# Optimization experiments

Measured on AMD Instinct MI355X. Metric: run time of the kernel, lower is better.

## Reference

```python
import jax, jax.numpy as jnp
import numpy as np
from jax import lax

ORDER = 6
WN = 0.5 / 50.0          # highpass_cutoff / (orig_fs/2)
UP, DOWN = 16, 25        # 64/100 reduced by gcd 4 (scipy resample_poly)
HALF_LEN = 10 * DOWN     # scipy kaiser half length = 10*max_rate
NTAPS = 2 * HALF_LEN + 1
PADLEN = 21              # sosfiltfilt default: 3*(2*n_sections+1), 3 biquads
CHANNELS = np.array([126, 125, 48, 112, 67, 93, 10, 61, 39, 108])
D_MODEL = 16
LN_EPS = 1e-5


def _butter_hp_sos(order, wn):
    # scipy.signal.butter(order, wn, btype='high', output='sos') in pure numpy
    fs = 2.0
    warped = 2.0 * fs * np.tan(np.pi * wn / fs)
    m = np.arange(-order + 1, order, 2)
    p = -np.exp(1j * np.pi * m / (2 * order))     # analog LP prototype poles
    k = np.real(1.0 / np.prod(-p))                # lp2hp gain (no zeros)
    p = warped / p                                # lp2hp poles; zeros at s=0
    z = np.zeros(order)
    fs2 = 2.0 * fs                                # bilinear, fs=2
    k = k * np.real(np.prod(fs2 - z) / np.prod(fs2 - p))
    z = (fs2 + z) / (fs2 - z)                     # digital zeros, all +1
    p = (fs2 + p) / (fs2 - p)
    pp = p[np.imag(p) > 0]
    pp = pp[np.argsort(-np.abs(np.abs(pp) - 1.0))]  # closest to unit circle last
    sos = []
    for i, pi in enumerate(pp):
        b = np.array([1.0, -2.0, 1.0]) * (k if i == 0 else 1.0)
        a = np.array([1.0, -2.0 * pi.real, np.abs(pi) ** 2])
        sos.append(np.concatenate([b, a]))
    return np.array(sos)


def _sosfilt_zi(sos):
    # scipy.signal.sosfilt_zi: steady-state of step response per section
    n = sos.shape[0]
    zi = np.zeros((n, 2))
    scale = 1.0
    for s in range(n):
        b0, b1, b2, _, a1, a2 = sos[s]
        A = np.array([[1.0 + a1, -1.0], [a2, 1.0]])
        B = np.array([b1 - a1 * b0, b2 - a2 * b0])
        zi[s] = scale * np.linalg.solve(A, B)
        scale *= (b0 + b1 + b2) / (1.0 + a1 + a2)
    return zi


SOS = _butter_hp_sos(ORDER, WN)
ZI = _sosfilt_zi(SOS)


def _resample_fir():
    # scipy firwin(2*half_len+1, 1/max_rate, window=('kaiser',5.0)) * up
    fc = 1.0 / DOWN
    m = np.arange(NTAPS) - (NTAPS - 1) / 2.0
    h = fc * np.sinc(fc * m) * np.kaiser(NTAPS, 5.0)
    h /= h.sum()
    return h * UP


H_BASE = _resample_fir()


def _pos_encoding(max_len, d):
    pos = np.arange(max_len)[:, None].astype(np.float64)
    div = np.exp(np.arange(0, d, 2) * (-np.log(10000.0) / d))
    pe = np.zeros((max_len, d))
    pe[:, 0::2] = np.sin(pos * div)
    pe[:, 1::2] = np.cos(pos * div)
    return pe.astype(np.float32)


PE = _pos_encoding(3840, D_MODEL)


def _sosfilt(x, zi):
    # x: (N,T), zi: (N,3,2). Cascade of biquads, transposed direct form II.
    sos = jnp.asarray(SOS, x.dtype)
    nsec = SOS.shape[0]

    def step(z, xt):
        v = xt
        zs = []
        for s in range(nsec):  # fixed tiny cascade, unrolled inside scan
            b0, b1, b2, a1, a2 = sos[s, 0], sos[s, 1], sos[s, 2], sos[s, 4], sos[s, 5]
            y = b0 * v + z[s][0]
            zs.append((b1 * v - a1 * y + z[s][1], b2 * v - a2 * y))
            v = y
        return tuple(zs), v

    z0 = tuple((zi[:, s, 0], zi[:, s, 1]) for s in range(nsec))
    _, y = lax.scan(step, z0, x.T)
    return y.T


def _sosfiltfilt(x):
    # scipy.signal.sosfiltfilt with default odd padding, padlen=21
    zi = jnp.asarray(ZI, x.dtype)
    front = 2.0 * x[:, :1] - x[:, PADLEN:0:-1]
    back = 2.0 * x[:, -1:] - x[:, -2:-PADLEN - 2:-1]
    ext = jnp.concatenate([front, x, back], axis=1)
    y = _sosfilt(ext, zi[None] * ext[:, 0, None, None])
    y = y[:, ::-1]
    y = _sosfilt(y, zi[None] * y[:, 0, None, None])
    return y[:, ::-1][:, PADLEN:-PADLEN]


def _resample_poly(x):
    # scipy.signal.resample_poly(x, 64, 100): upfirdn via dilated conv
    T = x.shape[-1]
    n_out = (T * UP) // DOWN + int((T * UP) % DOWN != 0)
    n_pre_pad = DOWN - HALF_LEN % DOWN
    n_pre_remove = (HALF_LEN + n_pre_pad) // DOWN

    def outlen(lh):
        return (((T - 1) * UP + lh) - 1) // DOWN + 1

    n_post = 0
    while outlen(NTAPS + n_pre_pad + n_post) < n_out + n_pre_remove:
        n_post += 1
    h = np.concatenate([np.zeros(n_pre_pad), H_BASE, np.zeros(n_post)])
    L = h.size
    rhs = jnp.asarray(h[::-1].copy(), x.dtype).reshape(1, 1, L)
    y = lax.conv_general_dilated(x[:, None, :], rhs, window_strides=(DOWN,),
                                 padding=[(L - 1, L - 1)], lhs_dilation=(UP,),
                                 dimension_numbers=('NCH', 'OIH', 'NCH'))
    return y[:, 0, n_pre_remove:n_pre_remove + n_out]


def _ln(x, g, b):
    mu = x.mean(-1, keepdims=True)
    var = ((x - mu) ** 2).mean(-1, keepdims=True)
    return (x - mu) * lax.rsqrt(var + LN_EPS) * g + b


def setup_inputs() -> dict:
    key = jax.random.key(0)
    ks = jax.random.split(key, 20)
    f32 = jnp.float32
    d = {
        'x': jax.random.normal(ks[0], (64, 128, 2000), f32),
        'conv_w': jax.random.normal(ks[1], (16, 10, 3), f32) * 0.15,
        'conv_b': jnp.zeros((16,), f32),
        'ln0_g': jnp.ones((16,), f32), 'ln0_b': jnp.zeros((16,), f32),
        'wqkv': jax.random.normal(ks[2], (48, 16), f32) * 0.125,
        'bqkv': jnp.zeros((48,), f32),
        'wo': jax.random.normal(ks[3], (16, 16), f32) * 0.25,
        'bo': jnp.zeros((16,), f32),
        'w1': jax.random.normal(ks[4], (32, 16), f32) * 0.2,
        'b1': jnp.zeros((32,), f32),
        'w2': jax.random.normal(ks[5], (16, 32), f32) * 0.2,
        'b2': jnp.zeros((16,), f32),
        'ln1_g': jnp.ones((16,), f32), 'ln1_b': jnp.zeros((16,), f32),
        'ln2_g': jnp.ones((16,), f32), 'ln2_b': jnp.zeros((16,), f32),
        'wfc': jax.random.normal(ks[6], (1, 16), f32) * 0.3,
        'bfc': jnp.zeros((1,), f32),
    }
    return d


def reference(x, conv_w, conv_b, ln0_g, ln0_b, wqkv, bqkv, wo, bo,
              w1, b1, w2, b2, ln1_g, ln1_b, ln2_g, ln2_b, wfc, bfc):
    B = x.shape[0]
    # remove Cz (last channel) then gather interesting channels
    x = x[:, :-1, :][:, jnp.asarray(CHANNELS), :]        # (B,10,T)
    x = x - x.mean(axis=1, keepdims=True)                # CAR
    C, T = x.shape[1], x.shape[2]
    xf = _sosfiltfilt(x.reshape(B * C, T))               # zero-phase highpass
    xr = _resample_poly(xf)                              # 100 Hz -> 64 Hz
    x = xr.reshape(B, C, -1)
    x = jnp.tanh(x)                                      # artifact_scale = 1.0
    mean = x.mean(axis=2, keepdims=True)                 # zscore, unbiased std
    var = ((x - mean) ** 2).sum(axis=2, keepdims=True) / (x.shape[2] - 1)
    std = jnp.maximum(jnp.sqrt(var), 1e-6)
    x = (x - mean) / std
    # conv1d k=3 pad=1 (10 -> 16) + relu
    x = lax.conv_general_dilated(x, conv_w, (1,), [(1, 1)],
                                 dimension_numbers=('NCH', 'OIH', 'NCH'))
    x = jax.nn.relu(x + conv_b[None, :, None])
    x = x.transpose(0, 2, 1)                             # (B,S,16)
    x = _ln(x, ln0_g, ln0_b)
    x = x + jnp.asarray(PE[:x.shape[1]], x.dtype)[None]
    # TransformerEncoderLayer, post-norm, nhead=1, relu FFN (eval: no dropout)
    qkv = x @ wqkv.T + bqkv
    q, k, v = jnp.split(qkv, 3, axis=-1)
    att = jax.nn.softmax(jnp.einsum('bqd,bkd->bqk', q, k) * 0.25, axis=-1)
    a = jnp.einsum('bqk,bkd->bqd', att, v) @ wo.T + bo
    x = _ln(x + a, ln1_g, ln1_b)
    f = jax.nn.relu(x @ w1.T + b1) @ w2.T + b2
    x = _ln(x + f, ln2_g, ln2_b)
    pooled = x.mean(axis=1)                              # adaptive avg pool -> 1
    return pooled @ wfc.T + bfc                          # (B,1)
```

## Files before the change

kernel.cpp:

```cpp
#include <hip/hip_runtime.h>
#include <cmath>
#include <complex>
#include <algorithm>

#ifndef M_PI
#define M_PI 3.14159265358979323846
#endif

typedef _Float16 f16x8 __attribute__((ext_vector_type(8)));
typedef _Float16 f16x4 __attribute__((ext_vector_type(4)));
typedef float f32x4 __attribute__((ext_vector_type(4)));

struct FiltArg {
  double b0[3], b1[3], b2[3], a1[3], a2[3];
  double zi0[3], zi1[3];
};
struct CorArg { double CA[16 * 6]; };
struct EigArg {
  double Pm[36], Pinv[36];
  double czi[6];
  double lam_re[3], lam_im[3];
  double lami_re[3], lami_im[3];
};
struct FirArg { float h[526]; };

static void design_sos(FiltArg& sa) {
  const int order = 6;
  const double wn = 0.5 / 50.0;
  const double fs = 2.0;
  double warped = 2.0 * fs * std::tan(M_PI * wn / fs);
  std::complex<double> p[6];
  for (int i = 0; i < order; i++) {
    int m = -order + 1 + 2 * i;
    p[i] = -std::exp(std::complex<double>(0.0, M_PI * m / (2.0 * order)));
  }
  std::complex<double> prod1(1, 0);
  for (int i = 0; i < 6; i++) prod1 *= -p[i];
  double k = (1.0 / prod1).real();
  for (int i = 0; i < 6; i++) p[i] = warped / p[i];
  const double fs2 = 2.0 * fs;
  std::complex<double> num(1, 0), den(1, 0);
  for (int i = 0; i < 6; i++) { num *= fs2; den *= (fs2 - p[i]); }
  k *= (num / den).real();
  for (int i = 0; i < 6; i++) p[i] = (fs2 + p[i]) / (fs2 - p[i]);
  std::complex<double> pp[3]; int n = 0;
  for (int i = 0; i < 6; i++) if (p[i].imag() > 0) pp[n++] = p[i];
  std::stable_sort(pp, pp + 3,
    [](const std::complex<double>& A, const std::complex<double>& B) {
      return std::fabs(std::abs(A) - 1.0) > std::fabs(std::abs(B) - 1.0);
    });
  double sos[3][6];
  for (int s = 0; s < 3; s++) {
    double g = (s == 0) ? k : 1.0;
    sos[s][0] = g; sos[s][1] = -2.0 * g; sos[s][2] = g;
    sos[s][3] = 1.0; sos[s][4] = -2.0 * pp[s].real(); sos[s][5] = std::norm(pp[s]);
  }
  double scale = 1.0;
  for (int s = 0; s < 3; s++) {
    double b0 = sos[s][0], b1 = sos[s][1], b2 = sos[s][2];
    double a1 = sos[s][4], a2 = sos[s][5];
    double det = 1.0 + a1 + a2;
    double r0 = b1 - a1 * b0, r1 = b2 - a2 * b0;
    double z0 = (r0 + r1) / det;
    double z1 = ((1.0 + a1) * r1 - a2 * r0) / det;
    sa.b0[s] = b0; sa.b1[s] = b1; sa.b2[s] = b2; sa.a1[s] = a1; sa.a2[s] = a2;
    sa.zi0[s] = scale * z0; sa.zi1[s] = scale * z1;
    scale *= (b0 + b1 + b2) / (1.0 + a1 + a2);
  }
}

static double host_step(const FiltArg& c, double z[6], double v) {
  for (int s = 0; s < 3; s++) {
    double y = c.b0[s] * v + z[2 * s];
    z[2 * s]     = c.b1[s] * v - c.a1[s] * y + z[2 * s + 1];
    z[2 * s + 1] = c.b2[s] * v - c.a2[s] * y;
    v = y;
  }
  return v;
}

static void build_filt(FiltArg& c, CorArg& co) {
  design_sos(c);
  for (int j = 0; j < 6; j++) {
    double z[6] = {0, 0, 0, 0, 0, 0};
    z[j] = 1.0;
    for (int i = 0; i < 16; i++) co.CA[i * 6 + j] = host_step(c, z, 0.0);
  }
}

static void build_eig(const FiltArg& c, EigArg& e) {
  double Pr[36];
  for (int s = 0; s < 3; s++) {
    double a1 = c.a1[s], a2 = c.a2[s];
    std::complex<double> disc = std::sqrt(std::complex<double>(a1 * a1 - 4.0 * a2, 0.0));
    std::complex<double> p = (-a1 + disc) / 2.0;
    if (p.imag() < 0) p = std::conj(p);
    std::complex<double> v[6] = {0, 0, 0, 0, 0, 0};
    v[2 * s] = 1.0;
    v[2 * s + 1] = a1 + p;
    std::complex<double> y = 1.0;
    for (int j = s + 1; j < 3; j++) {
      double b0j = c.b0[j], b1j = c.b1[j], b2j = c.b2[j];
      double a1j = c.a1[j], a2j = c.a2[j];
      std::complex<double> det = p * p + a1j * p + a2j;
      std::complex<double> r0 = (b1j - a1j * b0j) * y;
      std::complex<double> r1 = (b2j - a2j * b0j) * y;
      std::complex<double> z0 = (p * r0 + r1) / det;
      std::complex<double> z1 = ((p + a1j) * r1 - a2j * r0) / det;
      v[2 * j] = z0; v[2 * j + 1] = z1;
      y = b0j * y + z0;
    }
    for (int i = 0; i < 6; i++) {
      Pr[i * 6 + 2 * s]     = v[i].real();
      Pr[i * 6 + 2 * s + 1] = v[i].imag();
    }
    std::complex<double> lam = std::pow(p, 16);
    e.lam_re[s] = lam.real(); e.lam_im[s] = lam.imag();
    std::complex<double> li = 1.0 / lam;
    e.lami_re[s] = li.real(); e.lami_im[s] = li.imag();
  }
  for (int i = 0; i < 36; i++) e.Pm[i] = Pr[i];
  double M[6][12];
  for (int i = 0; i < 6; i++)
    for (int j = 0; j < 6; j++) { M[i][j] = Pr[i * 6 + j]; M[i][6 + j] = (i == j) ? 1.0 : 0.0; }
  for (int col = 0; col < 6; col++) {
    int piv = col;
    for (int i = col + 1; i < 6; i++)
      if (std::fabs(M[i][col]) > std::fabs(M[piv][col])) piv = i;
    if (piv != col) for (int j = 0; j < 12; j++) std::swap(M[col][j], M[piv][j]);
    double d = M[col][col];
    for (int j = 0; j < 12; j++) M[col][j] /= d;
    for (int i = 0; i < 6; i++) if (i != col) {
      double f = M[i][col];
      for (int j = 0; j < 12; j++) M[i][j] -= f * M[col][j];
    }
  }
  for (int i = 0; i < 6; i++)
    for (int j = 0; j < 6; j++) e.Pinv[i * 6 + j] = M[i][6 + j];
  double zv[6];
  for (int s = 0; s < 3; s++) { zv[2 * s] = c.zi0[s]; zv[2 * s + 1] = c.zi1[s]; }
  for (int i = 0; i < 6; i++) {
    double sum = 0.0;
    for (int j = 0; j < 6; j++) sum += e.Pinv[i * 6 + j] * zv[j];
    e.czi[i] = sum;
  }
}

static double bessel_i0(double x) {
  double s = 1.0, t = 1.0;
  for (int k = 1; k < 64; k++) {
    double u = x / (2.0 * k);
    t *= u * u; s += t;
    if (t < 1e-18 * s) break;
  }
  return s;
}

static void design_fir(FirArg& fa) {
  double h[501];
  const double fc = 1.0 / 25.0;
  double denom = bessel_i0(5.0);
  double sum = 0.0;
  for (int nn = 0; nn < 501; nn++) {
    double m = nn - 250.0;
    double xx = fc * m;
    double snc = (nn == 250) ? 1.0 : std::sin(M_PI * xx) / (M_PI * xx);
    double r = (2.0 * nn) / 500.0 - 1.0;
    double w = bessel_i0(5.0 * std::sqrt(std::max(0.0, 1.0 - r * r))) / denom;
    h[nn] = fc * snc * w; sum += h[nn];
  }
  for (int nn = 0; nn < 25; nn++) fa.h[nn] = 0.0f;
  for (int nn = 0; nn < 501; nn++) fa.h[25 + nn] = (float)(h[nn] / sum * 16.0);
}

__device__ inline double waveReduceSum(double v) {
  #pragma unroll
  for (int off = 32; off > 0; off >>= 1) v += __shfl_down(v, off, 64);
  return v;
}

__device__ inline void cpow_int(double br, double bi, int n, double& rr_, double& ri_) {
  double rr = 1.0, ri = 0.0;
  while (n) {
    if (n & 1) { double t = rr * br - ri * bi; ri = rr * bi + ri * br; rr = t; }
    double t2 = br * br - bi * bi; bi = 2.0 * br * bi; br = t2;
    n >>= 1;
  }
  rr_ = rr; ri_ = ri;
}

__global__ __launch_bounds__(256) void k_chansel_pe(const float* __restrict__ x,
                                                    float* __restrict__ xs,
                                                    float* __restrict__ pe,
                                                    float* __restrict__ out) {
  int gid = blockIdx.x;
  if (gid < 500) {
    int idx = gid * 256 + threadIdx.x;
    int b = idx / 2000, t = idx % 2000;
    const int ch[10] = {126, 125, 48, 112, 67, 93, 10, 61, 39, 108};
    const float* xb = x + (size_t)b * 128 * 2000;
    float v[10]; float s = 0.f;
    #pragma unroll
    for (int c = 0; c < 10; c++) { v[c] = xb[ch[c] * 2000 + t]; s += v[c]; }
    s *= 0.1f;
    #pragma unroll
    for (int c = 0; c < 10; c++) xs[((size_t)b * 10 + c) * 2000 + t] = v[c] - s;
  } else {
    int i = (gid - 500) * 256 + threadIdx.x;
    int t = i >> 4, d = i & 15, j = d >> 1;
    double div = exp(-((double)(2 * j)) * 0.5756462732485114);
    double a = (double)t * div;
    pe[i] = (float)((d & 1) ? cos(a) : sin(a));
    if (gid == 579 && threadIdx.x < 64) out[threadIdx.x] = 0.f;
  }
}

#define XR(t) xr[(t) + ((t) >> 5)]
#define YF(t) yf[(t) + ((t) >> 5)]
__global__ __launch_bounds__(128) void k_filtfilt(float* __restrict__ xs,
                                                  FiltArg c, CorArg co, EigArg eg) {
  __shared__ float xr[2112];
  __shared__ double yf[2112];
  __shared__ double wsum[3][2];
  int r = blockIdx.x;
  int gk = threadIdx.x;
  int lane = gk & 63;
  int wv = gk >> 6;
  float* x = xs + (size_t)r * 2000;

  float x0f = x[0], xlf = x[1999];
  for (int t = gk; t < 2048; t += 128) {
    float v;
    if (t < 21)        v = 2.f * x0f - x[21 - t];
    else if (t < 2021) v = x[t - 21];
    else if (t < 2042) v = 2.f * xlf - x[4019 - t];
    else               v = 0.f;
    XR(t) = v;
  }
  __syncthreads();

  double b0[3], b1[3], b2[3], a1[3], a2[3];
  #pragma unroll
  for (int s = 0; s < 3; s++) {
    b0[s] = c.b0[s]; b1[s] = c.b1[s]; b2[s] = c.b2[s];
    a1[s] = c.a1[s]; a2[s] = c.a2[s];
  }
  auto step = [&](double* z, double v) -> double {
    #pragma unroll
    for (int s = 0; s < 3; s++) {
      double y = b0[s] * v + z[2 * s];
      z[2 * s]     = b1[s] * v - a1[s] * y + z[2 * s + 1];
      z[2 * s + 1] = b2[s] * v - a2[s] * y;
      v = y;
    }
    return v;
  };

  auto eigscan = [&](double seed, const double* F, double* zst) {
    double G[6];
    #pragma unroll
    for (int i = 0; i < 6; i++) {
      double s = 0.0;
      #pragma unroll
      for (int j = 0; j < 6; j++) s += eg.Pinv[i * 6 + j] * F[j];
      G[i] = s;
    }
    double tre[3], tim[3], sre[3], sim[3];
    #pragma unroll
    for (int s3 = 0; s3 < 3; s3++) {
      double gre = G[2 * s3], gim = -G[2 * s3 + 1];
      double mre, mim;
      cpow_int(eg.lami_re[s3], eg.lami_im[s3], gk, mre, mim);
      tre[s3] = mre * gre - mim * gim;
      tim[s3] = mre * gim + mim * gre;
      double pr = tre[s3], pi = tim[s3];
      #pragma unroll
      for (int off = 1; off < 64; off <<= 1) {
        double ore = __shfl_up(pr, off, 64);
        double oim = __shfl_up(pi, off, 64);
        pr += (lane >= off) ? ore : 0.0;
        pi += (lane >= off) ? oim : 0.0;
      }
      sre[s3] = pr; sim[s3] = pi;
      if (wv == 0 && lane == 63) { wsum[s3][0] = pr; wsum[s3][1] = pi; }
    }
    __syncthreads();
    double coord[6];
    #pragma unroll
    for (int s3 = 0; s3 < 3; s3++) {
      double inc_re = sre[s3] + (wv ? wsum[s3][0] : 0.0);
      double inc_im = sim[s3] + (wv ? wsum[s3][1] : 0.0);
      double Sre = inc_re - tre[s3], Sim = inc_im - tim[s3];
      double c0re = seed * eg.czi[2 * s3];
      double c0im = -seed * eg.czi[2 * s3 + 1];
      double lkre, lkim;
      cpow_int(eg.lam_re[s3], eg.lam_im[s3], gk, lkre, lkim);
      double lm1re = lkre * eg.lami_re[s3] - lkim * eg.lami_im[s3];
      double lm1im = lkre * eg.lami_im[s3] + lkim * eg.lami_re[s3];
      if (gk == 0) { lm1re = 0.0; lm1im = 0.0; }
      double cre = lkre * c0re - lkim * c0im + lm1re * Sre - lm1im * Sim;
      double cim = lkre * c0im + lkim * c0re + lm1re * Sim + lm1im * Sre;
      coord[2 * s3] = cre;
      coord[2 * s3 + 1] = -cim;
    }
    #pragma unroll
    for (int i = 0; i < 6; i++) {
      double s = 0.0;
      #pragma unroll
      for (int j = 0; j < 6; j++) s += eg.Pm[i * 6 + j] * coord[j];
      zst[i] = s;
    }
  };

  int t0 = gk * 16;
  double z[6], yreg[16], zst[6];

  #pragma unroll
  for (int i = 0; i < 6; i++) z[i] = 0.0;
  for (int i = 0; i < 16; i++) yreg[i] = step(z, (double)XR(t0 + i));
  eigscan((double)XR(0), z, zst);
  for (int i = 0; i < 16; i++) {
    double corr = 0.0;
    #pragma unroll
    for (int j = 0; j < 6; j++) corr += co.CA[i * 6 + j] * zst[j];
    YF(t0 + i) = yreg[i] + corr;
  }
  __syncthreads();

  auto rin = [&](int j) -> double { return (j <= 2041) ? YF(2041 - j) : 0.0; };
  double seedB = YF(2041);
  #pragma unroll
  for (int i = 0; i < 6; i++) z[i] = 0.0;
  for (int i = 0; i < 16; i++) yreg[i] = step(z, rin(t0 + i));
  eigscan(seedB, z, zst);
  for (int i = 0; i < 16; i++) {
    int j = t0 + i;
    if (j >= 21 && j <= 2020) {
      double corr = 0.0;
      #pragma unroll
      for (int jj = 0; jj < 6; jj++) corr += co.CA[i * 6 + jj] * zst[jj];
      x[2020 - j] = (float)(yreg[i] + corr);
    }
  }
}

__global__ __launch_bounds__(256) void k_resample_norm(const float* __restrict__ xf,
                                                       float* __restrict__ xn,
                                                       FirArg fa) {
  __shared__ float xl[2000];
  __shared__ float hl[526];
  int r = blockIdx.x;
  const float* x = xf + (size_t)r * 2000;
  for (int i = threadIdx.x; i < 2000; i += 256) xl[i] = x[i];
  for (int i = threadIdx.x; i < 526; i += 256) hl[i] = fa.h[i];
  __syncthreads();
  float vals[5];
  #pragma unroll
  for (int kk = 0; kk < 5; kk++) {
    int o = threadIdx.x + kk * 256;
    int P = 25 * (o + 11);
    int phase = P & 15;
    float acc = 0.f;
    for (int m = phase; m <= 525; m += 16) {
      int idx = (P - m) >> 4;
      if (idx >= 0 && idx < 2000) acc += hl[m] * xl[idx];
    }
    vals[kk] = tanhf(acc);
  }
  double s = 0.0, ss = 0.0;
  #pragma unroll
  for (int kk = 0; kk < 5; kk++) {
    s += (double)vals[kk]; ss += (double)vals[kk] * (double)vals[kk];
  }
  s = waveReduceSum(s); ss = waveReduceSum(ss);
  __shared__ double red[8];
  int wid = threadIdx.x >> 6, lane = threadIdx.x & 63;
  if (lane == 0) { red[wid] = s; red[4 + wid] = ss; }
  __syncthreads();
  double S = red[0] + red[1] + red[2] + red[3];
  double SS = red[4] + red[5] + red[6] + red[7];
  double mean = S / 1280.0;
  double var = (SS - 1280.0 * mean * mean) / 1279.0;
  double sd = fmax(sqrt(fmax(var, 0.0)), 1e-6);
  float fmean = (float)mean, finv = (float)(1.0 / sd);
  #pragma unroll
  for (int kk = 0; kk < 5; kk++)
    xn[(size_t)r * 1280 + threadIdx.x + kk * 256] = (vals[kk] - fmean) * finv;
}

__global__ __launch_bounds__(256) void k_conv_ln_pe_qkv(const float* __restrict__ xn,
    const float* __restrict__ cw, const float* __restrict__ cb,
    const float* __restrict__ g0, const float* __restrict__ bt0,
    const float* __restrict__ wqkv, const float* __restrict__ bqkv,
    const float* __restrict__ pe,
    float* __restrict__ x0,
    float* __restrict__ Q, float* __restrict__ K, float* __restrict__ V) {
  __shared__ float w[480], bias[16], gg[16], gb[16];
  __shared__ float wq[768], bq[48];
  for (int i = threadIdx.x; i < 480; i += 256) w[i] = cw[i];
  for (int i = threadIdx.x; i < 768; i += 256) wq[i] = wqkv[i];
  if (threadIdx.x < 16) {
    bias[threadIdx.x] = cb[threadIdx.x];
    gg[threadIdx.x] = g0[threadIdx.x];
    gb[threadIdx.x] = bt0[threadIdx.x];
  }
  if (threadIdx.x < 48) bq[threadIdx.x] = bqkv[threadIdx.x];
  __syncthreads();
  int idx = blockIdx.x * 256 + threadIdx.x;
  int b = idx / 1280, t = idx % 1280;
  const float* xb = xn + (size_t)b * 10 * 1280;
  float in[10][3];
  #pragma unroll
  for (int i = 0; i < 10; i++)
    #pragma unroll
    for (int k = 0; k < 3; k++) {
      int tt = t - 1 + k;
      in[i][k] = (tt >= 0 && tt < 1280) ? xb[i * 1280 + tt] : 0.f;
    }
  float o[16];
  #pragma unroll
  for (int oc = 0; oc < 16; oc++) {
    float a = bias[oc];
    #pragma unroll
    for (int i = 0; i < 10; i++)
      #pragma unroll
      for (int k = 0; k < 3; k++) a += in[i][k] * w[oc * 30 + i * 3 + k];
    o[oc] = fmaxf(a, 0.f);
  }
  float mu = 0.f;
  #pragma unroll
  for (int d = 0; d < 16; d++) mu += o[d];
  mu *= (1.f / 16.f);
  float var = 0.f;
  #pragma unroll
  for (int d = 0; d < 16; d++) { float dd = o[d] - mu; var += dd * dd; }
  var *= (1.f / 16.f);
  float inv = 1.f / sqrtf(var + 1e-5f);
  float xv[16];
  float* outp = x0 + (size_t)idx * 16;
  const float* pep = pe + t * 16;
  #pragma unroll
  for (int d = 0; d < 16; d++) {
    xv[d] = (o[d] - mu) * inv * gg[d] + gb[d] + pep[d];
    outp[d] = xv[d];
  }
  float* qp = Q + (size_t)idx * 16;
  float* kp = K + (size_t)idx * 16;
  float* vp = V + (size_t)idx * 16;
  #pragma unroll
  for (int j = 0; j < 16; j++) {
    float a = bq[j];
    #pragma unroll
    for (int d = 0; d < 16; d++) a += xv[d] * wq[j * 16 + d];
    qp[j] = a;
  }
  #pragma unroll
  for (int j = 0; j < 16; j++) {
    float a = bq[16 + j];
    #pragma unroll
    for (int d = 0; d < 16; d++) a += xv[d] * wq[(16 + j) * 16 + d];
    kp[j] = a;
  }
  #pragma unroll
  for (int j = 0; j < 16; j++) {
    float a = bq[32 + j];
    #pragma unroll
    for (int d = 0; d < 16; d++) a += xv[d] * wq[(32 + j) * 16 + d];
    vp[j] = a;
  }
}

#define ATT_SHIFT 12.0f
__global__ __launch_bounds__(256) void k_attn_mfma(const float* __restrict__ Q,
    const float* __restrict__ K, const float* __restrict__ V,
    float* __restrict__ A) {
  __shared__ __align__(16) _Float16 Ks[64 * 40];
  __shared__ __align__(16) _Float16 Vt[16 * 72];
  __shared__ __align__(16) _Float16 Pld[4][16 * 40];
  int tid = threadIdx.x;
  int b  = blockIdx.x / 20;
  int rg = blockIdx.x % 20;
  int wv = tid >> 6;
  int lane = tid & 63;
  int col = lane & 15;
  int quad = lane >> 4;
  size_t base = (size_t)b * 1280;
  int row0 = rg * 64 + wv * 16;

  f16x8 qf;
  #pragma unroll
  for (int j = 0; j < 8; j++) qf[j] = (_Float16)0.f;
  if (quad < 2) {
    const float* qp = Q + (base + row0 + col) * 16 + quad * 8;
    #pragma unroll
    for (int j = 0; j < 8; j++) qf[j] = (_Float16)(0.25f * qp[j]);
  }
  f32x4 oacc = {0.f, 0.f, 0.f, 0.f};
  float lacc = 0.f;

  for (int s = 0; s < 20; s++) {
    __syncthreads();
    {
      int key = tid >> 2, part = tid & 3;
      const float* kp = K + (base + s * 64 + key) * 16 + part * 4;
      f16x4 hk, hz;
      #pragma unroll
      for (int j = 0; j < 4; j++) { hk[j] = (_Float16)kp[j]; hz[j] = (_Float16)0.f; }
      *(f16x4*)&Ks[key * 40 + part * 4] = hk;
      *(f16x4*)&Ks[key * 40 + 16 + part * 4] = hz;
      const float* vp = V + (base + s * 64 + key) * 16 + part * 4;
      #pragma unroll
      for (int j = 0; j < 4; j++) Vt[(part * 4 + j) * 72 + key] = (_Float16)vp[j];
    }
    __syncthreads();
    #pragma unroll
    for (int c = 0; c < 2; c++) {
      #pragma unroll
      for (int t = 0; t < 2; t++) {
        int keyoff = c * 32 + t * 16;
        f16x8 af = *(f16x8*)&Ks[(keyoff + col) * 40 + quad * 8];
        f32x4 sf = {0.f, 0.f, 0.f, 0.f};
        sf = __builtin_amdgcn_mfma_f32_16x16x32_f16(af, qf, sf, 0, 0, 0);
        f16x4 ph;
        float psum = 0.f;
        #pragma unroll
        for (int r = 0; r < 4; r++) {
          float p = __expf(sf[r] - ATT_SHIFT);
          psum += p;
          ph[r] = (_Float16)p;
        }
        lacc += psum;
        *(f16x4*)&Pld[wv][col * 40 + t * 16 + quad * 4] = ph;
      }
      __syncthreads();
      f16x8 pf = *(f16x8*)&Pld[wv][col * 40 + quad * 8];
      f16x8 vf = *(f16x8*)&Vt[col * 72 + c * 32 + quad * 8];
      oacc = __builtin_amdgcn_mfma_f32_16x16x32_f16(pf, vf, oacc, 0, 0, 0);
      __syncthreads();
    }
  }
  lacc += __shfl_xor(lacc, 16, 64);
  lacc += __shfl_xor(lacc, 32, 64);
  #pragma unroll
  for (int r = 0; r < 4; r++) {
    float lr = __shfl(lacc, quad * 4 + r, 64);
    A[(base + row0 + quad * 4 + r) * 16 + col] = oacc[r] / lr;
  }
}

__global__ __launch_bounds__(256) void k_combine_pool(
    const float* __restrict__ A, const float* __restrict__ x0,
    const float* __restrict__ wo, const float* __restrict__ bo,
    const float* __restrict__ w1, const float* __restrict__ b1,
    const float* __restrict__ w2, const float* __restrict__ b2,
    const float* __restrict__ g1, const float* __restrict__ bb1,
    const float* __restrict__ g2, const float* __restrict__ bb2,
    const float* __restrict__ wfc, const float* __restrict__ bfc,
    float* __restrict__ out) {
  __shared__ float swo[256], sw1[512], sw2[512];
  __shared__ float sbo[16], sb1[32], sb2[16], sg1[16], sbb1[16], sg2[16], sbb2[16];
  __shared__ float swf[16];
  int tid = threadIdx.x;
  swo[tid] = wo[tid];
  for (int i = tid; i < 512; i += 256) { sw1[i] = w1[i]; sw2[i] = w2[i]; }
  if (tid < 16) {
    sbo[tid] = bo[tid]; sb2[tid] = b2[tid];
    sg1[tid] = g1[tid]; sbb1[tid] = bb1[tid];
    sg2[tid] = g2[tid]; sbb2[tid] = bb2[tid];
    swf[tid] = wfc[tid];
  }
  if (tid < 32) sb1[tid] = b1[tid];
  __syncthreads();

  int idx = blockIdx.x * 256 + tid;
  int bb = blockIdx.x / 5;
  const float* pa = A + (size_t)idx * 16;
  float a[16];
  #pragma unroll
  for (int d = 0; d < 16; d++) a[d] = pa[d];
  float h[16];
  const float* xr = x0 + (size_t)idx * 16;
  #pragma unroll
  for (int d = 0; d < 16; d++) {
    float o = sbo[d];
    #pragma unroll
    for (int e = 0; e < 16; e++) o += a[e] * swo[d * 16 + e];
    h[d] = xr[d] + o;
  }
  float mu = 0.f;
  #pragma unroll
  for (int d = 0; d < 16; d++) mu += h[d];
  mu *= (1.f / 16.f);
  float var = 0.f;
  #pragma unroll
  for (int d = 0; d < 16; d++) { float dd = h[d] - mu; var += dd * dd; }
  var *= (1.f / 16.f);
  float inv = 1.f / sqrtf(var + 1e-5f);
  float x1[16];
  #pragma unroll
  for (int d = 0; d < 16; d++) x1[d] = (h[d] - mu) * inv * sg1[d] + sbb1[d];
  float t1[32];
  #pragma unroll
  for (int j = 0; j < 32; j++) {
    float u = sb1[j];
    #pragma unroll
    for (int d = 0; d < 16; d++) u += x1[d] * sw1[j * 16 + d];
    t1[j] = fmaxf(u, 0.f);
  }
  float h2[16];
  #pragma unroll
  for (int d = 0; d < 16; d++) {
    float u = sb2[d];
    #pragma unroll
    for (int j = 0; j < 32; j++) u += t1[j] * sw2[d * 32 + j];
    h2[d] = x1[d] + u;
  }
  mu = 0.f;
  #pragma unroll
  for (int d = 0; d < 16; d++) mu += h2[d];
  mu *= (1.f / 16.f);
  var = 0.f;
  #pragma unroll
  for (int d = 0; d < 16; d++) { float dd = h2[d] - mu; var += dd * dd; }
  var *= (1.f / 16.f);
  inv = 1.f / sqrtf(var + 1e-5f);
  float pv = 0.f;
  #pragma unroll
  for (int d = 0; d < 16; d++)
    pv += ((h2[d] - mu) * inv * sg2[d] + sbb2[d]) * swf[d];
  double part = waveReduceSum((double)pv);
  __shared__ double red[4];
  int wid = tid >> 6, lane = tid & 63;
  if (lane == 0) red[wid] = part;
  __syncthreads();
  if (tid == 0) {
    double S = red[0] + red[1] + red[2] + red[3];
    float add = (float)(S / 1280.0);
    if (blockIdx.x % 5 == 0) add += bfc[0];
    atomicAdd(&out[bb], add);
  }
}

extern "C" void kernel_launch(void* const* d_in, const int* in_sizes, int n_in,
                              void* d_out, int out_size, void* d_ws, size_t ws_size,
                              hipStream_t stream) {
  const float* x    = (const float*)d_in[0];
  const float* cw   = (const float*)d_in[1];
  const float* cb   = (const float*)d_in[2];
  const float* g0   = (const float*)d_in[3];
  const float* bt0  = (const float*)d_in[4];
  const float* wqkv = (const float*)d_in[5];
  const float* bqkv = (const float*)d_in[6];
  const float* wo   = (const float*)d_in[7];
  const float* bo   = (const float*)d_in[8];
  const float* w1   = (const float*)d_in[9];
  const float* b1   = (const float*)d_in[10];
  const float* w2   = (const float*)d_in[11];
  const float* b2   = (const float*)d_in[12];
  const float* g1   = (const float*)d_in[13];
  const float* bb1  = (const float*)d_in[14];
  const float* g2   = (const float*)d_in[15];
  const float* bb2  = (const float*)d_in[16];
  const float* wfc  = (const float*)d_in[17];
  const float* bfc  = (const float*)d_in[18];
  float* out = (float*)d_out;

  float* ws = (float*)d_ws;
  float* xs = ws;
  float* y1 = xs + 1280000;
  float* xn = y1 + 1306880;
  float* x0 = xn + 819200;
  float* Q  = x0 + 1310720;
  float* Kb = Q  + 1310720;
  float* Vb = Kb + 1310720;
  float* pe = Vb + 1310720;
  float* Abuf = ws;

  FiltArg fc; CorArg co; EigArg eg; FirArg fa;
  build_filt(fc, co);
  build_eig(fc, eg);
  design_fir(fa);

  k_chansel_pe<<<580, 256, 0, stream>>>(x, xs, pe, out);
  k_filtfilt<<<640, 128, 0, stream>>>(xs, fc, co, eg);
  k_resample_norm<<<640, 256, 0, stream>>>(xs, xn, fa);
  k_conv_ln_pe_qkv<<<320, 256, 0, stream>>>(xn, cw, cb, g0, bt0, wqkv, bqkv,
                                            pe, x0, Q, Kb, Vb);
  k_attn_mfma<<<1280, 256, 0, stream>>>(Q, Kb, Vb, Abuf);
  k_combine_pool<<<320, 256, 0, stream>>>(Abuf, x0, wo, bo, w1, b1, w2, b2,
                                          g1, bb1, g2, bb2, wfc, bfc, out);
}
```

Baseline: 242.8 us.

## Store K and transposed V as fp16 in producer to simplify attention tile loads

The QKV kernel now writes K as fp16 rows zero-padded to 32 halves and V as fp16 in a transposed per-batch layout. The attention kernel can then fill its shared tiles with single 16-byte vector copies, with no per-element conversion, transpose or zero fill. This cuts global traffic for K and V and removes repeated conversion work across the 20 row-group blocks that reload the same keys. The costs are strided 2-byte V stores in the producer and a 32-half K row stride in shared memory, which may cause bank conflicts where the old stride was 40.

```diff
diff --git a/kernel.cpp b/kernel.cpp
--- a/kernel.cpp
+++ b/kernel.cpp
@@ -393,8 +393,8 @@
     const float* __restrict__ g0, const float* __restrict__ bt0,
     const float* __restrict__ wqkv, const float* __restrict__ bqkv,
     const float* __restrict__ pe,
-    float* __restrict__ x0,
-    float* __restrict__ Q, float* __restrict__ K, float* __restrict__ V) {
+    float* __restrict__ x0, float* __restrict__ Q,
+    _Float16* __restrict__ Kp, _Float16* __restrict__ Vt_g) {
   __shared__ float w[480], bias[16], gg[16], gb[16];
   __shared__ float wq[768], bq[48];
   for (int i = threadIdx.x; i < 480; i += 256) w[i] = cw[i];
@@ -445,8 +445,6 @@
     outp[d] = xv[d];
   }
   float* qp = Q + (size_t)idx * 16;
-  float* kp = K + (size_t)idx * 16;
-  float* vp = V + (size_t)idx * 16;
   #pragma unroll
   for (int j = 0; j < 16; j++) {
     float a = bq[j];
@@ -454,27 +452,38 @@
     for (int d = 0; d < 16; d++) a += xv[d] * wq[j * 16 + d];
     qp[j] = a;
   }
-  #pragma unroll
-  for (int j = 0; j < 16; j++) {
-    float a = bq[16 + j];
-    #pragma unroll
-    for (int d = 0; d < 16; d++) a += xv[d] * wq[(16 + j) * 16 + d];
-    kp[j] = a;
-  }
-  #pragma unroll
-  for (int j = 0; j < 16; j++) {
-    float a = bq[32 + j];
-    #pragma unroll
-    for (int d = 0; d < 16; d++) a += xv[d] * wq[(32 + j) * 16 + d];
-    vp[j] = a;
+  {
+    _Float16* kp = Kp + (size_t)idx * 32;
+    #pragma unroll
+    for (int j = 0; j < 16; j++) {
+      float a = bq[16 + j];
+      #pragma unroll
+      for (int d = 0; d < 16; d++) a += xv[d] * wq[(16 + j) * 16 + d];
+      kp[j] = (_Float16)a;
+    }
+    f16x8 zz;
+    #pragma unroll
+    for (int j = 0; j < 8; j++) zz[j] = (_Float16)0.f;
+    *(f16x8*)&kp[16] = zz;
+    *(f16x8*)&kp[24] = zz;
+  }
+  {
+    _Float16* vt = Vt_g + (size_t)b * 16 * 1280 + t;
+    #pragma unroll
+    for (int j = 0; j < 16; j++) {
+      float a = bq[32 + j];
+      #pragma unroll
+      for (int d = 0; d < 16; d++) a += xv[d] * wq[(32 + j) * 16 + d];
+      vt[j * 1280] = (_Float16)a;
+    }
   }
 }
 
 #define ATT_SHIFT 12.0f
 __global__ __launch_bounds__(256) void k_attn_mfma(const float* __restrict__ Q,
-    const float* __restrict__ K, const float* __restrict__ V,
+    const _Float16* __restrict__ Kp, const _Float16* __restrict__ Vt_g,
     float* __restrict__ A) {
-  __shared__ __align__(16) _Float16 Ks[64 * 40];
+  __shared__ __align__(16) _Float16 Ks2[64 * 32];
   __shared__ __align__(16) _Float16 Vt[16 * 72];
   __shared__ __align__(16) _Float16 Pld[4][16 * 40];
   int tid = threadIdx.x;
@@ -498,19 +507,16 @@
   f32x4 oacc = {0.f, 0.f, 0.f, 0.f};
   float lacc = 0.f;
 
+  const _Float16* vt_b = Vt_g + (size_t)b * 16 * 1280;
+
   for (int s = 0; s < 20; s++) {
     __syncthreads();
-    {
-      int key = tid >> 2, part = tid & 3;
-      const float* kp = K + (base + s * 64 + key) * 16 + part * 4;
-      f16x4 hk, hz;
-      #pragma unroll
-      for (int j = 0; j < 4; j++) { hk[j] = (_Float16)kp[j]; hz[j] = (_Float16)0.f; }
-      *(f16x4*)&Ks[key * 40 + part * 4] = hk;
-      *(f16x4*)&Ks[key * 40 + 16 + part * 4] = hz;
-      const float* vp = V + (base + s * 64 + key) * 16 + part * 4;
-      #pragma unroll
-      for (int j = 0; j < 4; j++) Vt[(part * 4 + j) * 72 + key] = (_Float16)vp[j];
+    *(f16x8*)&Ks2[tid * 8] =
+        *(const f16x8*)(Kp + (base + s * 64) * 32 + tid * 8);
+    if (tid < 128) {
+      int d = tid >> 3, qc = tid & 7;
+      *(f16x8*)&Vt[d * 72 + qc * 8] =
+          *(const f16x8*)(vt_b + d * 1280 + s * 64 + qc * 8);
     }
     __syncthreads();
     #pragma unroll
@@ -518,7 +524,7 @@
       #pragma unroll
       for (int t = 0; t < 2; t++) {
         int keyoff = c * 32 + t * 16;
-        f16x8 af = *(f16x8*)&Ks[(keyoff + col) * 40 + quad * 8];
+        f16x8 af = *(f16x8*)&Ks2[(keyoff + col) * 32 + quad * 8];
         f32x4 sf = {0.f, 0.f, 0.f, 0.f};
         sf = __builtin_amdgcn_mfma_f32_16x16x32_f16(af, qf, sf, 0, 0, 0);
         f16x4 ph;
@@ -671,9 +677,9 @@
   float* xn = y1 + 1306880;
   float* x0 = xn + 819200;
   float* Q  = x0 + 1310720;
-  float* Kb = Q  + 1310720;
-  float* Vb = Kb + 1310720;
-  float* pe = Vb + 1310720;
+  _Float16* Kp   = (_Float16*)(Q + 1310720);
+  _Float16* Vt_g = (_Float16*)(Q + 2621440);
+  float* pe = Q + 2621440 + 655360;
   float* Abuf = ws;
 
   FiltArg fc; CorArg co; EigArg eg; FirArg fa;
@@ -685,8 +691,8 @@
   k_filtfilt<<<640, 128, 0, stream>>>(xs, fc, co, eg);
   k_resample_norm<<<640, 256, 0, stream>>>(xs, xn, fa);
   k_conv_ln_pe_qkv<<<320, 256, 0, stream>>>(xn, cw, cb, g0, bt0, wqkv, bqkv,
-                                            pe, x0, Q, Kb, Vb);
-  k_attn_mfma<<<1280, 256, 0, stream>>>(Q, Kb, Vb, Abuf);
+                                            pe, x0, Q, Kp, Vt_g);
+  k_attn_mfma<<<1280, 256, 0, stream>>>(Q, Kp, Vt_g, Abuf);
   k_combine_pool<<<320, 256, 0, stream>>>(Abuf, x0, wo, bo, w1, b1, w2, b2,
                                           g1, bb1, g2, bb2, wfc, bfc, out);
 }
```

Result: faster. 235.5 us (-3.0%).
